# Performance work log

Measured on AMD Instinct MI355X. Metric: run time of the kernel, lower is better.

Reference implementation:

```python
import jax, jax.numpy as jnp
import numpy as np

N, E, DIN, HID, G, L = 50000, 200000, 128, 128, 64, 6
H1, H2 = 8, 4
EPS_LN, EPS_BN = 1e-5, 1e-5


def setup_inputs() -> dict:
    key = jax.random.key(0)
    ks = iter(jax.random.split(key, 32))
    def nrm(shape, scale=0.05):
        return jax.random.normal(next(ks), shape, dtype=jnp.float32) * scale
    z = lambda *s: jnp.zeros(s, jnp.float32)
    o = lambda *s: jnp.ones(s, jnp.float32)
    return {
        'x': jax.random.normal(next(ks), (N, DIN), dtype=jnp.float32),
        'edge_index': jax.random.randint(next(ks), (2, E), 0, N),
        'batch': jnp.sort(jax.random.randint(next(ks), (N,), 0, G)),
        'W1': nrm((DIN, H1 * HID)), 'a_src1': nrm((H1, HID)), 'a_dst1': nrm((H1, HID)), 'b1': z(H1 * HID),
        'W2': nrm((H1 * HID, H2 * HID)), 'a_src2': nrm((H2, HID)), 'a_dst2': nrm((H2, HID)), 'b2': z(H2 * HID),
        'W3': nrm((H2 * HID, HID)), 'b3': z(HID),
        'wq': nrm((L, HID, HID)), 'bq': z(L, HID), 'wk': nrm((L, HID, HID)), 'bk': z(L, HID),
        'wv': nrm((L, HID, HID)), 'bv': z(L, HID), 'wo': nrm((L, HID, HID)), 'bo': z(L, HID),
        'ln1g': o(L, HID), 'ln1b': z(L, HID), 'ln2g': o(L, HID), 'ln2b': z(L, HID),
        'wf1': nrm((L, HID, 4 * HID)), 'bf1': z(L, 4 * HID), 'wf2': nrm((L, 4 * HID, HID)), 'bf2': z(L, HID),
        'bn1_g': o(2 * HID), 'bn1_b': z(2 * HID),
        'fc1_w': nrm((2 * HID, HID // 2)), 'fc1_b': z(HID // 2),
        'bn2_g': o(HID // 2), 'bn2_b': z(HID // 2),
        'fc2_w': nrm((HID // 2, 2)), 'fc2_b': z(2),
    }


def _ln(x, g, b):
    mu = x.mean(-1, keepdims=True)
    v = ((x - mu) ** 2).mean(-1, keepdims=True)
    return (x - mu) * jax.lax.rsqrt(v + EPS_LN) * g + b


def _gat(x, src, dst, W, a_s, a_d, b, heads):
    # PyG GATConv: message src -> dst, segment softmax over incoming edges per dst.
    h = (x @ W).reshape(x.shape[0], heads, -1)           # [N, H, C]
    e = jax.nn.leaky_relu((h * a_s).sum(-1)[src] + (h * a_d).sum(-1)[dst], 0.2)  # [E, H]
    m = jax.ops.segment_max(e, dst, num_segments=N)
    ex = jnp.exp(e - jnp.where(jnp.isfinite(m), m, 0.0)[dst])
    s = jax.ops.segment_sum(ex, dst, num_segments=N)
    alpha = ex / (s[dst] + 1e-16)
    out = jax.ops.segment_sum(alpha[:, :, None] * h[src], dst, num_segments=N)
    return out.reshape(N, -1) + b


def _forward(x, edge_index, batch, W1, a_src1, a_dst1, b1, W2, a_src2, a_dst2, b2, W3, b3,
             wq, bq, wk, bk, wv, bv, wo, bo, ln1g, ln1b, ln2g, ln2b, wf1, bf1, wf2, bf2,
             bn1_g, bn1_b, fc1_w, fc1_b, bn2_g, bn2_b, fc2_w, fc2_b):
    loop = jnp.arange(N, dtype=edge_index.dtype)
    src = jnp.concatenate([edge_index[0], loop])          # add self-loops (PyG default)
    dst = jnp.concatenate([edge_index[1], loop])
    h = jax.nn.elu(_gat(x, src, dst, W1, a_src1, a_dst1, b1, H1))
    h = jax.nn.elu(_gat(h, src, dst, W2, a_src2, a_dst2, b2, H2))
    # GCNConv with symmetric normalization (self-loops already included)
    deg = jax.ops.segment_sum(jnp.ones(src.shape, h.dtype), dst, num_segments=N)
    dinv = jnp.where(deg > 0, jax.lax.rsqrt(jnp.maximum(deg, 1e-12)), 0.0)
    norm = dinv[src] * dinv[dst]
    h = jax.nn.elu(jax.ops.segment_sum(norm[:, None] * (h @ W3)[src], dst, num_segments=N) + b3)
    # TransformerEncoder over seq_len=1 (h3.unsqueeze(1)): softmax over one key == 1,
    # so MHA output == Wo @ (Wv h + bv) + bo exactly; q/k have no effect on the output.
    for l in range(L):
        sa = (h @ wv[l] + bv[l]) @ wo[l] + bo[l]
        h = _ln(h + sa, ln1g[l], ln1b[l])
        ff = jax.nn.gelu(h @ wf1[l] + bf1[l], approximate=False) @ wf2[l] + bf2[l]
        h = _ln(h + ff, ln2g[l], ln2b[l])
    # global mean / max pool over graphs
    cnt = jax.ops.segment_sum(jnp.ones((N,), h.dtype), batch, num_segments=G)
    hm = jax.ops.segment_sum(h, batch, num_segments=G) / jnp.maximum(cnt, 1.0)[:, None]
    hx = jax.ops.segment_max(h, batch, num_segments=G)
    hx = jnp.where(jnp.isfinite(hx), hx, 0.0)
    hc = jnp.concatenate([hm, hx], axis=1)                # [G, 2*HID]
    bn_s = 1.0 / np.sqrt(1.0 + EPS_BN)                    # eval BN: running stats (0, 1)
    hc = hc * bn_s * bn1_g + bn1_b
    hc = jax.nn.elu(hc @ fc1_w + fc1_b)
    hc = hc * bn_s * bn2_g + bn2_b
    return hc @ fc2_w + fc2_b                             # [G, 2]


def reference(x, edge_index, batch, W1, a_src1, a_dst1, b1, W2, a_src2, a_dst2, b2, W3, b3,
              wq, bq, wk, bk, wv, bv, wo, bo, ln1g, ln1b, ln2g, ln2b, wf1, bf1, wf2, bf2,
              bn1_g, bn1_b, fc1_w, fc1_b, bn2_g, bn2_b, fc2_w, fc2_b):
    return _forward(x, edge_index, batch, W1, a_src1, a_dst1, b1, W2, a_src2, a_dst2, b2, W3, b3,
                    wq, bq, wk, bk, wv, bv, wo, bo, ln1g, ln1b, ln2g, ln2b, wf1, bf1, wf2, bf2,
                    bn1_g, bn1_b, fc1_w, fc1_b, bn2_g, bn2_b, fc2_w, fc2_b)
```

## Files before the change

### kernel.cpp

```cpp
#include <hip/hip_runtime.h>
#include <hip/hip_bf16.h>
#include <math.h>

#define NN 50000
#define EE 200000
#define ET 250000
#define GG 64
#define LL 6

using short8 = __attribute__((ext_vector_type(8))) short;
using f32x4  = __attribute__((ext_vector_type(4))) float;
typedef unsigned short ushortT;

__device__ __forceinline__ float elu1(float x) { return x > 0.f ? x : expm1f(x); }
__device__ __forceinline__ float gelu_exact(float x) {
    return 0.5f * x * (1.f + erff(x * 0.70710678118654752440f));
}
__device__ __forceinline__ short f2bf(float f) {
    __hip_bfloat16 h = __float2bfloat16(f);
    return *reinterpret_cast<short*>(&h);
}
__device__ __forceinline__ float bf2f(ushortT u) {
    return __uint_as_float(((unsigned)u) << 16);
}
__device__ __forceinline__ void accum8(float* acc, float a, uint4 d) {
    acc[0] += a * bf2f((ushortT)(d.x & 0xffff));
    acc[1] += a * bf2f((ushortT)(d.x >> 16));
    acc[2] += a * bf2f((ushortT)(d.y & 0xffff));
    acc[3] += a * bf2f((ushortT)(d.y >> 16));
    acc[4] += a * bf2f((ushortT)(d.z & 0xffff));
    acc[5] += a * bf2f((ushortT)(d.z >> 16));
    acc[6] += a * bf2f((ushortT)(d.w & 0xffff));
    acc[7] += a * bf2f((ushortT)(d.w >> 16));
}

__global__ void count_deg_kernel(const int* __restrict__ ei, int* __restrict__ deg) {
    int e = blockIdx.x * 256 + threadIdx.x;
    if (e >= ET) return;
    int dst = (e < EE) ? ei[EE + e] : (e - EE);
    atomicAdd(&deg[dst], 1);
}

__global__ void scan_kernel(const int* __restrict__ deg, int* __restrict__ row_ptr, int n) {
    __shared__ int s[1024];
    int tid = threadIdx.x;
    const int per = (n + 1023) / 1024;
    int lo = tid * per, hi = min(lo + per, n);
    int sum = 0;
    for (int i = lo; i < hi; i++) sum += deg[i];
    s[tid] = sum;
    __syncthreads();
    for (int off = 1; off < 1024; off <<= 1) {
        int t = (tid >= off) ? s[tid - off] : 0;
        __syncthreads();
        s[tid] += t;
        __syncthreads();
    }
    int run = s[tid] - sum;
    for (int i = lo; i < hi; i++) { row_ptr[i] = run; run += deg[i]; }
    if (tid == 1023) row_ptr[n] = s[1023];
}

__global__ void fill_csr_kernel(const int* __restrict__ ei, const int* __restrict__ row_ptr,
                                int* __restrict__ cursor, int* __restrict__ edge_src) {
    int e = blockIdx.x * 256 + threadIdx.x;
    if (e >= ET) return;
    int src, dst;
    if (e < EE) { src = ei[e]; dst = ei[EE + e]; }
    else        { src = e - EE; dst = e - EE; }
    int pos = atomicAdd(&cursor[dst], 1);
    edge_src[row_ptr[dst] + pos] = src;
}

__global__ void dinv_kernel(const int* __restrict__ row_ptr, float* __restrict__ dinv) {
    int n = blockIdx.x * 256 + threadIdx.x;
    if (n >= NN) return;
    int d = row_ptr[n + 1] - row_ptr[n];
    dinv[n] = (d > 0) ? rsqrtf((float)d) : 0.f;
}

__global__ __launch_bounds__(256) void local_sort_kernel(
    const int* __restrict__ row_ptr, int* __restrict__ perm, int n_nodes) {
    int g = blockIdx.x * 4 + (threadIdx.x >> 6);
    int l = threadIdx.x & 63;
    int node = g * 64 + l;
    if (g * 64 >= n_nodes) return;
    int d = (node < n_nodes) ? (row_ptr[node + 1] - row_ptr[node]) : 0x7fffffff;
    int rank = 0;
#pragma unroll 16
    for (int j = 0; j < 64; j++) {
        int dj = __shfl(d, j);
        rank += (dj < d) || (dj == d && j < l);
    }
    if (node < n_nodes) perm[g * 64 + rank] = node;
}

__global__ void wvwo_kernel(const float* __restrict__ wv, const float* __restrict__ wo,
                            const float* __restrict__ bv, const float* __restrict__ bo,
                            float* __restrict__ Wvo, float* __restrict__ bvo) {
    int l = blockIdx.y;
    const float* Wv = wv + l * 16384;
    const float* Wo = wo + l * 16384;
    int tid = blockIdx.x * 256 + threadIdx.x;
    if (tid < 16384) {
        int r = tid >> 7, c = tid & 127;
        float s = 0.f;
        for (int k = 0; k < 128; k++) s += Wv[r * 128 + k] * Wo[k * 128 + c];
        Wvo[l * 16384 + tid] = s;
    }
    if (blockIdx.x == 0 && threadIdx.x < 128) {
        int c = threadIdx.x;
        float s = bo[l * 128 + c];
        for (int k = 0; k < 128; k++) s += bv[l * 128 + k] * Wo[k * 128 + c];
        bvo[l * 128 + c] = s;
    }
}

__global__ void bprep_kernel(const float* __restrict__ B, short* __restrict__ Bp,
                             int K, int N, int ldb, long srcStride) {
    int layer = blockIdx.y;
    const float* Bsrc = B + srcStride * layer;
    short* Bd = Bp + (size_t)K * N * layer;
    int total = (K >> 5) * (N >> 4) * 64;
    int tid = blockIdx.x * 256 + threadIdx.x;
    if (tid >= total) return;
    int l = tid & 63;
    int rest = tid >> 6;
    int kbc = K >> 5;
    int kb = rest % kbc;
    int c16 = rest / kbc;
    int n = c16 * 16 + (l & 15);
    int kbase = kb * 32 + (l >> 4) * 8;
    short v[8];
#pragma unroll
    for (int j = 0; j < 8; j++) v[j] = f2bf(Bsrc[(size_t)(kbase + j) * ldb + n]);
    *(uint4*)(Bd + (size_t)tid * 8) = *(uint4*)v;
}

__global__ void cast_bf16_kernel(const float* __restrict__ in, short* __restrict__ out, int n4) {
    int i = blockIdx.x * 256 + threadIdx.x;
    if (i >= n4) return;
    float4 v = *(const float4*)(in + (size_t)i * 4);
    short s[4] = { f2bf(v.x), f2bf(v.y), f2bf(v.z), f2bf(v.w) };
    *(uint2*)(out + (size_t)i * 4) = *(uint2*)s;
}

template <int EPI, bool BIAS, bool OUTBF16, int NSPLIT, int KBC,
          bool TMAJ = false, bool ATILE32 = false>
__global__ __launch_bounds__(256) void gemm_bf16_kernel(
    const short* __restrict__ A, const short* __restrict__ Bp,
    const float* __restrict__ bias, void* __restrict__ Cv,
    const float* __restrict__ a_s, const float* __restrict__ a_d,
    float* __restrict__ as_out, float* __restrict__ ad_out, int asH,
    const ushortT* __restrict__ Rres, const float* __restrict__ lng,
    const float* __restrict__ lnb, float* __restrict__ Qout,
    __hip_bfloat16* __restrict__ Qbout,
    int M, int K, int Nc) {
    __shared__ short Bs[(KBC > 0) ? KBC * 4096 : 8192];
    int t = threadIdx.x;
    int w = t >> 6, l = t & 63;
    int ln = l & 15, lq = l >> 4;
    int MBceil = (M + 63) >> 6;
    int bx = blockIdx.x;
    int xcd = bx & 7, idx = bx >> 3;
    int t2 = idx % NSPLIT;
    int mb = (idx / NSPLIT) * 8 + xcd;
    if (mb >= MBceil) return;
    int bm = mb * 64 + w * 16;
    int arow = bm + ln;
    bool aok = arow < M;
    int rowb = bm + lq * 4;
    const short* Ap = A + (size_t)arow * K + lq * 8;

    auto aload = [&](int kb) -> short8 {
        if (!aok) return (short8){0, 0, 0, 0, 0, 0, 0, 0};
        const short* p;
        if constexpr (ATILE32)
            p = A + ((size_t)kb * M + arow) * 32 + lq * 8;
        else
            p = Ap + kb * 32;
        return *(const short8*)p;
    };

    f32x4 acc[8];
#pragma unroll
    for (int j = 0; j < 8; j++) acc[j] = (f32x4){0.f, 0.f, 0.f, 0.f};

    if constexpr (KBC > 0) {
        {
            const uint4* src = (const uint4*)(Bp + (size_t)t2 * KBC * 4096);
            uint4* dst = (uint4*)Bs;
#pragma unroll
            for (int i = 0; i < KBC * 2; i++)
                dst[i * 256 + t] = src[i * 256 + t];
        }
        short8 af[KBC];
#pragma unroll
        for (int kb = 0; kb < KBC; kb++)
            af[kb] = aload(kb);
        __syncthreads();
#pragma unroll
        for (int kb = 0; kb < KBC; kb++)
#pragma unroll
            for (int ct = 0; ct < 8; ct++) {
                short8 bfr = *(const short8*)(Bs + ((ct * KBC + kb) * 64 + l) * 8);
                acc[ct] = __builtin_amdgcn_mfma_f32_16x16x32_bf16(af[kb], bfr, acc[ct], 0, 0, 0);
            }
    } else {
        int kbc = K >> 5;
        int sct = t >> 5, spart = t & 31;
        auto stage = [&](int buf, int kb) {
            const uint4* src = (const uint4*)(Bp + ((size_t)(t2 * 8 + sct) * kbc + kb) * 512);
            uint4* dst = (uint4*)(Bs + buf * 4096 + sct * 512);
            dst[spart * 2]     = src[spart * 2];
            dst[spart * 2 + 1] = src[spart * 2 + 1];
        };
        stage(0, 0);
        __syncthreads();
        for (int kb = 0; kb < kbc; kb++) {
            if (kb + 1 < kbc) stage((kb + 1) & 1, kb + 1);
            short8 af = aload(kb);
            const short* bsb = Bs + (kb & 1) * 4096;
#pragma unroll
            for (int ct = 0; ct < 8; ct++) {
                short8 bfr = *(const short8*)(bsb + (ct * 64 + l) * 8);
                acc[ct] = __builtin_amdgcn_mfma_f32_16x16x32_bf16(af, bfr, acc[ct], 0, 0, 0);
            }
            __syncthreads();
        }
    }

    if (EPI == 2) {
        const float* asv = a_s + t2 * 128;
        const float* adv = a_d + t2 * 128;
#pragma unroll
        for (int reg = 0; reg < 4; reg++) {
            float vs = 0.f, vd = 0.f;
#pragma unroll
            for (int ct = 0; ct < 8; ct++) {
                int colL = ct * 16 + ln;
                float av = acc[ct][reg];
                vs += av * asv[colL];
                vd += av * adv[colL];
            }
            vs += __shfl_xor(vs, 1); vs += __shfl_xor(vs, 2);
            vs += __shfl_xor(vs, 4); vs += __shfl_xor(vs, 8);
            vd += __shfl_xor(vd, 1); vd += __shfl_xor(vd, 2);
            vd += __shfl_xor(vd, 4); vd += __shfl_xor(vd, 8);
            int row = rowb + reg;
            if (ln == 0 && row < M) {
                as_out[(size_t)row * asH + t2] = vs;
                ad_out[(size_t)row * asH + t2] = vd;
            }
        }
    }
    if (EPI == 3) {
        float v[8][4];
#pragma unroll
        for (int ct = 0; ct < 8; ct++) {
            int col = ct * 16 + ln;
            float bv_ = bias[col];
#pragma unroll
            for (int reg = 0; reg < 4; reg++) {
                int row = rowb + reg;
                float r = (row < M) ? bf2f(Rres[(size_t)row * 128 + col]) : 0.f;
                v[ct][reg] = acc[ct][reg] + bv_ + r;
            }
        }
#pragma unroll
        for (int reg = 0; reg < 4; reg++) {
            float s = 0.f;
#pragma unroll
            for (int ct = 0; ct < 8; ct++) s += v[ct][reg];
            s += __shfl_xor(s, 1); s += __shfl_xor(s, 2);
            s += __shfl_xor(s, 4); s += __shfl_xor(s, 8);
            float mean = s * (1.f / 128.f);
            float s2 = 0.f;
#pragma unroll
            for (int ct = 0; ct < 8; ct++) { float d = v[ct][reg] - mean; s2 += d * d; }
            s2 += __shfl_xor(s2, 1); s2 += __shfl_xor(s2, 2);
            s2 += __shfl_xor(s2, 4); s2 += __shfl_xor(s2, 8);
            float rstd = rsqrtf(s2 * (1.f / 128.f) + 1e-5f);
            int row = rowb + reg;
            if (row < M) {
#pragma unroll
                for (int ct = 0; ct < 8; ct++) {
                    int col = ct * 16 + ln;
                    float o = (v[ct][reg] - mean) * rstd * lng[col] + lnb[col];
                    Qbout[(size_t)row * 128 + col] = __float2bfloat16(o);
                    if (Qout) Qout[(size_t)row * 128 + col] = o;
                }
            }
        }
    }
    if (EPI == 0 || EPI == 1 || EPI == 2) {
#pragma unroll
        for (int ct = 0; ct < 8; ct++) {
            int col = t2 * 128 + ct * 16 + ln;
            float bv_ = BIAS ? bias[col] : 0.f;
#pragma unroll
            for (int reg = 0; reg < 4; reg++) {
                int row = rowb + reg;
                if (row < M) {
                    float v = acc[ct][reg] + bv_;
                    if (EPI == 1) v = gelu_exact(v);
                    if (OUTBF16) {
                        size_t addr;
                        if constexpr (TMAJ)
                            addr = ((size_t)(col >> 5) * M + row) * 32 + (col & 31);
                        else
                            addr = (size_t)row * Nc + col;
                        ((__hip_bfloat16*)Cv)[addr] = __float2bfloat16(v);
                    } else {
                        ((float*)Cv)[(size_t)row * Nc + col] = v;
                    }
                }
            }
        }
    }
}

template <int H>
__global__ __launch_bounds__(256) void gat_alpha_kernel(
    const float* __restrict__ as_, const float* __restrict__ ad_,
    const int* __restrict__ row_ptr, const int* __restrict__ edge_src,
    float* __restrict__ exA, float* __restrict__ exS, int n_nodes) {
    const int GS = 64 / H;
    int node = blockIdx.x * 4 + (threadIdx.x >> 6);
    if (node >= n_nodes) return;
    int l = threadIdx.x & 63;
    int h = l / GS;
    int lig = l % GS;
    int start = row_ptr[node];
    int deg = row_ptr[node + 1] - start;
    float adn = ad_[(size_t)node * H + h];
    float m = -1e30f;
    for (int j = lig; j < deg; j += GS) {
        int s = edge_src[start + j];
        float e = as_[(size_t)s * H + h] + adn;
        e = e > 0.f ? e : 0.2f * e;
        m = fmaxf(m, e);
    }
#pragma unroll
    for (int mask = 1; mask < GS; mask <<= 1)
        m = fmaxf(m, __shfl_xor(m, mask));
    float S = 0.f;
    for (int j = lig; j < deg; j += GS) {
        int s = edge_src[start + j];
        float e = as_[(size_t)s * H + h] + adn;
        e = e > 0.f ? e : 0.2f * e;
        float ex = expf(e - m);
        exA[(size_t)h * ET + (start + j)] = ex;
        S += ex;
    }
#pragma unroll
    for (int mask = 1; mask < GS; mask <<= 1)
        S += __shfl_xor(S, mask);
    if (lig == 0) exS[(size_t)h * n_nodes + node] = S;
}

__global__ __launch_bounds__(256) void gat_agg_tiled_kernel(
    const ushortT* __restrict__ hT, const float* __restrict__ exA,
    const float* __restrict__ exS, const float* __restrict__ bias,
    const int* __restrict__ row_ptr, const int* __restrict__ edge_src,
    const int* __restrict__ perm,
    __hip_bfloat16* __restrict__ outT, int n_nodes, int NB) {
    int bx = blockIdx.x;
    int xcd = bx & 7, rest = bx >> 3;
    int tl = rest / NB, nb = rest - tl * NB;
    int tile = tl * 8 + xcd;
    int nl = threadIdx.x >> 2, q = threadIdx.x & 3;
    int idx = nb * 64 + nl;
    if (idx >= n_nodes) return;
    int node = perm[idx];
    int hb = tile >> 2;
    const ushortT* __restrict__ base = hT + (size_t)tile * n_nodes * 32 + q * 8;
    const float* __restrict__ exAh = exA + (size_t)hb * ET;
    int start = row_ptr[node];
    int deg = row_ptr[node + 1] - start;
    float acc[8];
#pragma unroll
    for (int c = 0; c < 8; c++) acc[c] = 0.f;
    for (int j = 0; j < deg; j++) {
        int s = edge_src[start + j];
        float a = exAh[start + j];
        uint4 d = *(const uint4*)(base + (size_t)s * 32);
        accum8(acc, a, d);
    }
    float inv = 1.f / (exS[(size_t)hb * n_nodes + node] + 1e-16f);
    const float* bp = bias + tile * 32 + q * 8;
    short o[8];
#pragma unroll
    for (int c = 0; c < 8; c++)
        o[c] = f2bf(elu1(acc[c] * inv + bp[c]));
    *(uint4*)(outT + ((size_t)tile * n_nodes + node) * 32 + q * 8) = *(uint4*)o;
}

__global__ __launch_bounds__(256, 2) void gcn_agg_kernel(
    const ushortT* __restrict__ hp, const float* __restrict__ dinv,
    const float* __restrict__ b3, const int* __restrict__ row_ptr,
    const int* __restrict__ edge_src,
    __hip_bfloat16* __restrict__ outb, int n_nodes) {
    int node = blockIdx.x * 2 + (threadIdx.x >> 7);
    int c = threadIdx.x & 127;
    if (node >= n_nodes) return;
    int start = row_ptr[node];
    int deg = row_ptr[node + 1] - start;
    float dn = dinv[node];
    float acc = 0.f;
    auto LS = [&](int j) { return edge_src[start + min(j, deg - 1)]; };
    int s0 = LS(0), s1 = LS(1), s2 = LS(2), s3 = LS(3);
    int s4 = LS(4), s5 = LS(5), s6 = LS(6), s7 = LS(7);
    auto HW = [&](int s, int j, float& h, float& w) {
        h = bf2f(hp[(size_t)s * 128 + c]);
        w = (j < deg) ? dinv[s] * dn : 0.f;
    };
    float h0, h1, h2, h3, h4, h5, h6, h7;
    float w0, w1, w2, w3, w4, w5, w6, w7;
    HW(s0, 0, h0, w0); HW(s1, 1, h1, w1); HW(s2, 2, h2, w2); HW(s3, 3, h3, w3);
    HW(s4, 4, h4, w4); HW(s5, 5, h5, w5); HW(s6, 6, h6, w6); HW(s7, 7, h7, w7);
    int j0 = 0;
    while (true) {
        int jn = j0 + 8;
        bool more = jn < deg;
        float g0, g1, g2, g3, g4, g5, g6, g7;
        float v0 = 0.f, v1 = 0.f, v2 = 0.f, v3 = 0.f;
        float v4 = 0.f, v5 = 0.f, v6 = 0.f, v7 = 0.f;
        if (more) {
            int t0 = LS(jn),     t1 = LS(jn + 1), t2 = LS(jn + 2), t3 = LS(jn + 3);
            int t4 = LS(jn + 4), t5 = LS(jn + 5), t6 = LS(jn + 6), t7 = LS(jn + 7);
            HW(t0, jn,     g0, v0); HW(t1, jn + 1, g1, v1);
            HW(t2, jn + 2, g2, v2); HW(t3, jn + 3, g3, v3);
            HW(t4, jn + 4, g4, v4); HW(t5, jn + 5, g5, v5);
            HW(t6, jn + 6, g6, v6); HW(t7, jn + 7, g7, v7);
        }
        acc += w0 * h0 + w1 * h1 + w2 * h2 + w3 * h3
             + w4 * h4 + w5 * h5 + w6 * h6 + w7 * h7;
        if (!more) break;
        h0 = g0; h1 = g1; h2 = g2; h3 = g3;
        h4 = g4; h5 = g5; h6 = g6; h7 = g7;
        w0 = v0; w1 = v1; w2 = v2; w3 = v3;
        w4 = v4; w5 = v5; w6 = v6; w7 = v7;
        j0 = jn;
    }
    outb[(size_t)node * 128 + c] = __float2bfloat16(elu1(acc + b3[c]));
}

__global__ void pool1_kernel(const float* __restrict__ Q, const int* __restrict__ batch,
                             float* __restrict__ psum, float* __restrict__ pmax, int n_nodes) {
    int g = blockIdx.x, seg = blockIdx.y;
    int c = threadIdx.x;
    int lo, hi;
    {
        int l = 0, h = n_nodes;
        while (l < h) { int mid = (l + h) >> 1; if (batch[mid] < g) l = mid + 1; else h = mid; }
        lo = l;
        l = lo; h = n_nodes;
        while (l < h) { int mid = (l + h) >> 1; if (batch[mid] < g + 1) l = mid + 1; else h = mid; }
        hi = l;
    }
    int len = hi - lo;
    int a = lo + (int)((long)len * seg / 8);
    int b = lo + (int)((long)len * (seg + 1) / 8);
    float s = 0.f, mx = -INFINITY;
    for (int n = a; n < b; n++) {
        float v = Q[(size_t)n * 128 + c];
        s += v;
        mx = fmaxf(mx, v);
    }
    psum[(g * 8 + seg) * 128 + c] = s;
    pmax[(g * 8 + seg) * 128 + c] = mx;
}

__global__ void pool2_kernel(const float* __restrict__ psum, const float* __restrict__ pmax,
                             const int* __restrict__ batch,
                             const float* __restrict__ bn1g, const float* __restrict__ bn1b,
                             float* __restrict__ hc, int n_nodes) {
    int g = blockIdx.x;
    int c = threadIdx.x;
    int lo, hi;
    {
        int l = 0, h = n_nodes;
        while (l < h) { int mid = (l + h) >> 1; if (batch[mid] < g) l = mid + 1; else h = mid; }
        lo = l;
        l = lo; h = n_nodes;
        while (l < h) { int mid = (l + h) >> 1; if (batch[mid] < g + 1) l = mid + 1; else h = mid; }
        hi = l;
    }
    int cnt = hi - lo;
    float s = 0.f, mx = -INFINITY;
    for (int seg = 0; seg < 8; seg++) {
        s += psum[(g * 8 + seg) * 128 + c];
        mx = fmaxf(mx, pmax[(g * 8 + seg) * 128 + c]);
    }
    float hm = s / fmaxf((float)cnt, 1.f);
    float hx = (cnt > 0 && isfinite(mx)) ? mx : 0.f;
    const float bn_s = 0.99999500003749968f;
    hc[g * 256 + c]       = hm * bn_s * bn1g[c] + bn1b[c];
    hc[g * 256 + 128 + c] = hx * bn_s * bn1g[128 + c] + bn1b[128 + c];
}

__global__ void head_kernel(const float* __restrict__ hc,
                            const float* __restrict__ fc1w, const float* __restrict__ fc1b,
                            const float* __restrict__ bn2g, const float* __restrict__ bn2b,
                            const float* __restrict__ fc2w, const float* __restrict__ fc2b,
                            float* __restrict__ out) {
    int g = blockIdx.x;
    int j = threadIdx.x;
    const float bn_s = 0.99999500003749968f;
    float acc = fc1b[j];
    for (int i = 0; i < 256; i++) acc += hc[g * 256 + i] * fc1w[i * 64 + j];
    acc = elu1(acc);
    acc = acc * bn_s * bn2g[j] + bn2b[j];
    __shared__ float sv[64];
    sv[j] = acc;
    __syncthreads();
    if (j < 2) {
        float o = fc2b[j];
        for (int i = 0; i < 64; i++) o += sv[i] * fc2w[i * 2 + j];
        out[g * 2 + j] = o;
    }
}

extern "C" void kernel_launch(void* const* d_in, const int* in_sizes, int n_in,
                              void* d_out, int out_size, void* d_ws, size_t ws_size,
                              hipStream_t stream) {
    const float* x    = (const float*)d_in[0];
    const int*   ei   = (const int*)d_in[1];
    const int*   batch= (const int*)d_in[2];
    const float* W1   = (const float*)d_in[3];
    const float* as1  = (const float*)d_in[4];
    const float* ad1  = (const float*)d_in[5];
    const float* b1   = (const float*)d_in[6];
    const float* W2   = (const float*)d_in[7];
    const float* as2  = (const float*)d_in[8];
    const float* ad2  = (const float*)d_in[9];
    const float* b2   = (const float*)d_in[10];
    const float* W3   = (const float*)d_in[11];
    const float* b3   = (const float*)d_in[12];
    const float* wv   = (const float*)d_in[17];
    const float* bv   = (const float*)d_in[18];
    const float* wo   = (const float*)d_in[19];
    const float* bo   = (const float*)d_in[20];
    const float* ln1g = (const float*)d_in[21];
    const float* ln1b = (const float*)d_in[22];
    const float* ln2g = (const float*)d_in[23];
    const float* ln2b = (const float*)d_in[24];
    const float* wf1  = (const float*)d_in[25];
    const float* bf1  = (const float*)d_in[26];
    const float* wf2  = (const float*)d_in[27];
    const float* bf2  = (const float*)d_in[28];
    const float* bn1g = (const float*)d_in[29];
    const float* bn1b = (const float*)d_in[30];
    const float* fc1w = (const float*)d_in[31];
    const float* fc1b = (const float*)d_in[32];
    const float* bn2g = (const float*)d_in[33];
    const float* bn2b = (const float*)d_in[34];
    const float* fc2w = (const float*)d_in[35];
    const float* fc2b = (const float*)d_in[36];
    float* out = (float*)d_out;

    char* wsb = (char*)d_ws;
    short* xb    = (short*)wsb;
    float* exAf  = (float*)wsb;
    float* exSf  = (float*)(wsb + 8000000);
    short* h1t   = (short*)(wsb + 12800000);
    short* h2t   = (short*)(wsb + 12800000);
    short* h3pre = (short*)(wsb + 12800000);
    short* FFb   = (short*)(wsb + 25600000);
    short* bh1   = (short*)(wsb + 115200000);
    short* bh2   = (short*)(wsb + 115200000);
    float* fQ    = (float*)(wsb + 128000000);
    short* Qb    = (short*)(wsb + 153600000);
    char* tail = wsb + 217600000;
    short* W1p  = (short*)tail;  tail += 262144;
    short* W2p  = (short*)tail;  tail += 1048576;
    short* W3p  = (short*)tail;  tail += 131072;
    short* Wvop = (short*)tail;  tail += 196608;
    short* wf1p = (short*)tail;  tail += 786432;
    short* wf2p = (short*)tail;  tail += 786432;
    float* Wvo  = (float*)tail;  tail += 393216;
    float* bvo  = (float*)tail;  tail += 3072;
    float* fAS  = (float*)tail;  tail += 1600000;
    float* fAD  = (float*)tail;  tail += 1600000;
    float* fDv  = (float*)tail;  tail += 200000;
    float* psum = (float*)tail;  tail += 262144;
    float* pmax = (float*)tail;  tail += 262144;
    float* fHC  = (float*)tail;  tail += 65536;
    int* iDeg   = (int*)tail;    tail += 200000;
    int* iRP    = (int*)tail;    tail += 200004;
    int* iCur   = (int*)tail;    tail += 200000;
    int* iES    = (int*)tail;    tail += 1000000;

    hipMemsetAsync(iDeg, 0, NN * sizeof(int), stream);
    hipMemsetAsync(iCur, 0, NN * sizeof(int), stream);

    count_deg_kernel<<<(ET + 255) / 256, 256, 0, stream>>>(ei, iDeg);
    scan_kernel<<<1, 1024, 0, stream>>>(iDeg, iRP, NN);
    fill_csr_kernel<<<(ET + 255) / 256, 256, 0, stream>>>(ei, iRP, iCur, iES);
    dinv_kernel<<<(NN + 255) / 256, 256, 0, stream>>>(iRP, fDv);
    int* perm = iCur;
    local_sort_kernel<<<(NN / 64 + 4) / 4, 256, 0, stream>>>(iRP, perm, NN);

    wvwo_kernel<<<dim3(64, 6), 256, 0, stream>>>(wv, wo, bv, bo, Wvo, bvo);
    auto bprep = [&](const float* B, short* Bp, int K, int N, int ldb, long sStride, int layers) {
        int total = (K >> 5) * (N >> 4) * 64;
        dim3 grid((total + 255) / 256, layers);
        bprep_kernel<<<grid, 256, 0, stream>>>(B, Bp, K, N, ldb, sStride);
    };
    bprep(W1, W1p, 128, 1024, 1024, 0, 1);
    bprep(W2, W2p, 1024, 512, 512, 0, 1);
    bprep(W3, W3p, 512, 128, 128, 0, 1);
    bprep(Wvo, Wvop, 128, 128, 128, 16384, 6);
    bprep(wf1, wf1p, 128, 512, 512, 65536, 6);
    bprep(wf2, wf2p, 512, 128, 128, 65536, 6);
    cast_bf16_kernel<<<(NN * 128 / 4 + 255) / 256, 256, 0, stream>>>(x, xb, NN * 128 / 4);

    const int MB64 = (NN + 63) / 64;
    const int MBp = ((MB64 + 7) / 8) * 8;
    const int NB = (NN + 63) / 64;

    gemm_bf16_kernel<2, false, true, 8, 4, true, false><<<MBp * 8, 256, 0, stream>>>(
        xb, W1p, nullptr, h1t, as1, ad1, fAS, fAD, 8,
        nullptr, nullptr, nullptr, nullptr, nullptr, NN, 128, 1024);
    gat_alpha_kernel<8><<<(NN + 3) / 4, 256, 0, stream>>>(
        fAS, fAD, iRP, iES, exAf, exSf, NN);
    gat_agg_tiled_kernel<<<4 * NB * 8, 256, 0, stream>>>(
        (const ushortT*)h1t, exAf, exSf, b1, iRP, iES, perm, (__hip_bfloat16*)bh1, NN, NB);
    gemm_bf16_kernel<2, false, true, 4, 0, true, true><<<MBp * 4, 256, 0, stream>>>(
        bh1, W2p, nullptr, h2t, as2, ad2, fAS, fAD, 4,
        nullptr, nullptr, nullptr, nullptr, nullptr, NN, 1024, 512);
    gat_alpha_kernel<4><<<(NN + 3) / 4, 256, 0, stream>>>(
        fAS, fAD, iRP, iES, exAf, exSf, NN);
    gat_agg_tiled_kernel<<<2 * NB * 8, 256, 0, stream>>>(
        (const ushortT*)h2t, exAf, exSf, b2, iRP, iES, perm, (__hip_bfloat16*)bh2, NN, NB);
    gemm_bf16_kernel<0, false, true, 1, 0, false, true><<<MBp, 256, 0, stream>>>(
        bh2, W3p, nullptr, h3pre, nullptr, nullptr, nullptr, nullptr, 0,
        nullptr, nullptr, nullptr, nullptr, nullptr, NN, 512, 128);
    gcn_agg_kernel<<<(NN + 1) / 2, 256, 0, stream>>>(
        (const ushortT*)h3pre, fDv, b3, iRP, iES, (__hip_bfloat16*)Qb, NN);
    for (int l = 0; l < LL; l++) {
        gemm_bf16_kernel<3, true, false, 1, 4><<<MBp, 256, 0, stream>>>(
            Qb, Wvop + l * 16384, bvo + l * 128, nullptr, nullptr, nullptr, nullptr, nullptr, 0,
            (const ushortT*)Qb, ln1g + l * 128, ln1b + l * 128, nullptr, (__hip_bfloat16*)Qb,
            NN, 128, 128);
        gemm_bf16_kernel<1, true, true, 4, 4><<<MBp * 4, 256, 0, stream>>>(
            Qb, wf1p + l * 65536, bf1 + l * 512, FFb, nullptr, nullptr, nullptr, nullptr, 0,
            nullptr, nullptr, nullptr, nullptr, nullptr, NN, 128, 512);
        gemm_bf16_kernel<3, true, false, 1, 0><<<MBp, 256, 0, stream>>>(
            FFb, wf2p + l * 65536, bf2 + l * 128, nullptr, nullptr, nullptr, nullptr, nullptr, 0,
            (const ushortT*)Qb, ln2g + l * 128, ln2b + l * 128,
            (l == LL - 1) ? fQ : nullptr, (__hip_bfloat16*)Qb, NN, 512, 128);
    }
    pool1_kernel<<<dim3(GG, 8), 128, 0, stream>>>(fQ, batch, psum, pmax, NN);
    pool2_kernel<<<GG, 128, 0, stream>>>(psum, pmax, batch, bn1g, bn1b, fHC, NN);
    head_kernel<<<GG, 64, 0, stream>>>(fHC, fc1w, fc1b, bn2g, bn2b, fc2w, fc2b, out);
}
```

Measured before the change: 1.299 ms.

## Fuse feed-forward up-projection, GELU, down-projection and LayerNorm into one kernel

Replaces the two per-layer FFN GEMM launches with a single kernel. It computes each 128-column chunk of the 512-wide GELU hidden activation into shared memory and immediately accumulates it into the down-projection, then applies the residual add and LayerNorm in registers. This removes the 50000x512 bf16 intermediate write and read per layer, plus one launch. In exchange, each block reloads both weight matrices through shared memory with more barriers, and occupancy is limited by about 49KB of LDS per block.

```diff
diff --git a/kernel.cpp b/kernel.cpp
--- a/kernel.cpp
+++ b/kernel.cpp
@@ -315,6 +315,124 @@
                         ((float*)Cv)[(size_t)row * Nc + col] = v;
                     }
                 }
+            }
+        }
+    }
+}
+
+__global__ __launch_bounds__(256) void ff_fused_kernel(
+    const short* __restrict__ Qb, const short* __restrict__ wf1p,
+    const short* __restrict__ wf2p, const float* __restrict__ bf1,
+    const float* __restrict__ bf2, const float* __restrict__ lng,
+    const float* __restrict__ lnb, float* __restrict__ Qout,
+    __hip_bfloat16* __restrict__ Qbout, int M) {
+    __shared__ short Bs[16384];
+    __shared__ short Ts[4][16 * 132];
+    int t = threadIdx.x;
+    int w = t >> 6, l = t & 63;
+    int ln = l & 15, lq = l >> 4;
+    int MBceil = (M + 63) >> 6;
+    int bx = blockIdx.x;
+    int xcd = bx & 7, mb = (bx >> 3) * 8 + xcd;
+    if (mb >= MBceil) return;
+    int bm = mb * 64 + w * 16;
+    int arow = bm + ln;
+    bool aok = arow < M;
+    int rowb = bm + lq * 4;
+
+    short8 af1[4];
+#pragma unroll
+    for (int kb = 0; kb < 4; kb++)
+        af1[kb] = aok ? *(const short8*)(Qb + (size_t)arow * 128 + kb * 32 + lq * 8)
+                      : (short8){0, 0, 0, 0, 0, 0, 0, 0};
+
+    f32x4 acc2[8];
+#pragma unroll
+    for (int j = 0; j < 8; j++) acc2[j] = (f32x4){0.f, 0.f, 0.f, 0.f};
+
+    short* Tw = &Ts[w][0];
+    for (int kc = 0; kc < 4; kc++) {
+        __syncthreads();
+        {
+            const uint4* src = (const uint4*)(wf1p + kc * 16384);
+            uint4* dst = (uint4*)Bs;
+#pragma unroll
+            for (int i = 0; i < 8; i++) dst[i * 256 + t] = src[i * 256 + t];
+        }
+        __syncthreads();
+        f32x4 acct[8];
+#pragma unroll
+        for (int j = 0; j < 8; j++) acct[j] = (f32x4){0.f, 0.f, 0.f, 0.f};
+#pragma unroll
+        for (int kb = 0; kb < 4; kb++)
+#pragma unroll
+            for (int ct = 0; ct < 8; ct++) {
+                short8 bfr = *(const short8*)(Bs + ((ct * 4 + kb) * 64 + l) * 8);
+                acct[ct] = __builtin_amdgcn_mfma_f32_16x16x32_bf16(af1[kb], bfr, acct[ct], 0, 0, 0);
+            }
+#pragma unroll
+        for (int ct = 0; ct < 8; ct++) {
+            float bv = bf1[kc * 128 + ct * 16 + ln];
+#pragma unroll
+            for (int reg = 0; reg < 4; reg++)
+                Tw[(lq * 4 + reg) * 132 + ct * 16 + ln] = f2bf(gelu_exact(acct[ct][reg] + bv));
+        }
+        __syncthreads();
+        {
+            int sct = t >> 5, spart = t & 31;
+            const uint4* src = (const uint4*)(wf2p + (size_t)(sct * 16 + kc * 4) * 512);
+            uint4* dst = (uint4*)Bs + sct * 256;
+#pragma unroll
+            for (int j = 0; j < 8; j++) dst[spart + j * 32] = src[spart + j * 32];
+        }
+        short8 a2[4];
+#pragma unroll
+        for (int kb2 = 0; kb2 < 4; kb2++)
+            a2[kb2] = *(const short8*)(Tw + ln * 132 + kb2 * 32 + lq * 8);
+        __syncthreads();
+#pragma unroll
+        for (int kb2 = 0; kb2 < 4; kb2++)
+#pragma unroll
+            for (int ct = 0; ct < 8; ct++) {
+                short8 bfr = *(const short8*)(Bs + ((ct * 4 + kb2) * 64 + l) * 8);
+                acc2[ct] = __builtin_amdgcn_mfma_f32_16x16x32_bf16(a2[kb2], bfr, acc2[ct], 0, 0, 0);
+            }
+    }
+
+    float v[8][4];
+#pragma unroll
+    for (int ct = 0; ct < 8; ct++) {
+        int col = ct * 16 + ln;
+        float bv_ = bf2[col];
+#pragma unroll
+        for (int reg = 0; reg < 4; reg++) {
+            int row = rowb + reg;
+            float r = (row < M) ? bf2f(((const ushortT*)Qb)[(size_t)row * 128 + col]) : 0.f;
+            v[ct][reg] = acc2[ct][reg] + bv_ + r;
+        }
+    }
+#pragma unroll
+    for (int reg = 0; reg < 4; reg++) {
+        float s = 0.f;
+#pragma unroll
+        for (int ct = 0; ct < 8; ct++) s += v[ct][reg];
+        s += __shfl_xor(s, 1); s += __shfl_xor(s, 2);
+        s += __shfl_xor(s, 4); s += __shfl_xor(s, 8);
+        float mean = s * (1.f / 128.f);
+        float s2 = 0.f;
+#pragma unroll
+        for (int ct = 0; ct < 8; ct++) { float d = v[ct][reg] - mean; s2 += d * d; }
+        s2 += __shfl_xor(s2, 1); s2 += __shfl_xor(s2, 2);
+        s2 += __shfl_xor(s2, 4); s2 += __shfl_xor(s2, 8);
+        float rstd = rsqrtf(s2 * (1.f / 128.f) + 1e-5f);
+        int row = rowb + reg;
+        if (row < M) {
+#pragma unroll
+            for (int ct = 0; ct < 8; ct++) {
+                int col = ct * 16 + ln;
+                float o = (v[ct][reg] - mean) * rstd * lng[col] + lnb[col];
+                Qbout[(size_t)row * 128 + col] = __float2bfloat16(o);
+                if (Qout) Qout[(size_t)row * 128 + col] = o;
             }
         }
     }
@@ -567,7 +685,6 @@
     short* h1t   = (short*)(wsb + 12800000);
     short* h2t   = (short*)(wsb + 12800000);
     short* h3pre = (short*)(wsb + 12800000);
-    short* FFb   = (short*)(wsb + 25600000);
     short* bh1   = (short*)(wsb + 115200000);
     short* bh2   = (short*)(wsb + 115200000);
     float* fQ    = (float*)(wsb + 128000000);
@@ -644,13 +761,10 @@
             Qb, Wvop + l * 16384, bvo + l * 128, nullptr, nullptr, nullptr, nullptr, nullptr, 0,
             (const ushortT*)Qb, ln1g + l * 128, ln1b + l * 128, nullptr, (__hip_bfloat16*)Qb,
             NN, 128, 128);
-        gemm_bf16_kernel<1, true, true, 4, 4><<<MBp * 4, 256, 0, stream>>>(
-            Qb, wf1p + l * 65536, bf1 + l * 512, FFb, nullptr, nullptr, nullptr, nullptr, 0,
-            nullptr, nullptr, nullptr, nullptr, nullptr, NN, 128, 512);
-        gemm_bf16_kernel<3, true, false, 1, 0><<<MBp, 256, 0, stream>>>(
-            FFb, wf2p + l * 65536, bf2 + l * 128, nullptr, nullptr, nullptr, nullptr, nullptr, 0,
-            (const ushortT*)Qb, ln2g + l * 128, ln2b + l * 128,
-            (l == LL - 1) ? fQ : nullptr, (__hip_bfloat16*)Qb, NN, 512, 128);
+        ff_fused_kernel<<<MBp, 256, 0, stream>>>(
+            Qb, wf1p + l * 65536, wf2p + l * 65536, bf1 + l * 512, bf2 + l * 128,
+            ln2g + l * 128, ln2b + l * 128,
+            (l == LL - 1) ? fQ : nullptr, (__hip_bfloat16*)Qb, NN);
     }
     pool1_kernel<<<dim3(GG, 8), 128, 0, stream>>>(fQ, batch, psum, pmax, NN);
     pool2_kernel<<<GG, 128, 0, stream>>>(psum, pmax, batch, bn1g, bn1b, fHC, NN);
```

New measurement: 1.331 ms. +2.4%, slower.
